# Performance work log

Measured on AMD Instinct MI355X. Metric: run time of the kernel, lower is better.

Reference implementation:

```python
import jax, jax.numpy as jnp
import numpy as np

B, T, D = 64, 512, 1024
V_TAG, V_TYPE = 6, 20
TAG_PAD, TYPE_PAD = 5, 19
E = 2048          # total entity spans in the batch (sliced cascade mode)
MAX_SPAN = 8      # max entity span length


def setup_inputs() -> dict:
    key = jax.random.key(0)
    ks = jax.random.split(key, 12)
    full_hidden = jax.random.normal(ks[0], (B, T, D), dtype=jnp.float32)
    W_tag = jax.random.normal(ks[1], (D, V_TAG), dtype=jnp.float32) * 0.02
    b_tag = jnp.zeros((V_TAG,), jnp.float32)
    W_type = jax.random.normal(ks[2], (D, V_TYPE), dtype=jnp.float32) * 0.02
    b_type = jnp.zeros((V_TYPE,), jnp.float32)
    crf_start = jax.random.normal(ks[3], (V_TAG,), dtype=jnp.float32) * 0.1
    crf_end = jax.random.normal(ks[4], (V_TAG,), dtype=jnp.float32) * 0.1
    crf_trans = jax.random.normal(ks[5], (V_TAG, V_TAG), dtype=jnp.float32) * 0.1
    # ragged sequence lengths (>= MAX_SPAN+1 so all positions/spans are sane)
    seq_lens = jnp.maximum(jax.random.randint(ks[6], (B,), 1, T + 1), MAX_SPAN + 1).astype(jnp.int32)
    tag_ids = jax.random.randint(ks[7], (B, T), 0, V_TAG - 1).astype(jnp.int32)  # exclude pad tag
    ent_sample_ids = jax.random.randint(ks[8], (E,), 0, B).astype(jnp.int32)
    ent_starts = jax.random.randint(ks[9], (E,), 0, T - MAX_SPAN).astype(jnp.int32)
    ent_lens = jax.random.randint(ks[10], (E,), 1, MAX_SPAN + 1)
    ent_ends = (ent_starts + ent_lens).astype(jnp.int32)
    ent_type_ids = jax.random.randint(ks[11], (E,), 0, V_TYPE - 1).astype(jnp.int32)  # exclude pad type
    return dict(full_hidden=full_hidden, W_tag=W_tag, b_tag=b_tag, W_type=W_type,
                b_type=b_type, crf_start=crf_start, crf_end=crf_end, crf_trans=crf_trans,
                tag_ids=tag_ids, seq_lens=seq_lens, ent_sample_ids=ent_sample_ids,
                ent_starts=ent_starts, ent_ends=ent_ends, ent_type_ids=ent_type_ids)


def reference(full_hidden, W_tag, b_tag, W_type, b_type, crf_start, crf_end, crf_trans,
              tag_ids, seq_lens, ent_sample_ids, ent_starts, ent_ends, ent_type_ids):
    mask = jnp.arange(T)[None, :] < seq_lens[:, None]                  # [B,T] bool (tok_mask)
    maskf = mask.astype(full_hidden.dtype)

    # ---- base CRF decoder: tag projection + CRF NLL per sample ----
    tag_feats = full_hidden @ W_tag + b_tag                            # [B,T,V_TAG]

    # gold path score
    emit_scores = jnp.take_along_axis(tag_feats, tag_ids[..., None].astype(jnp.int32), axis=-1)[..., 0]  # [B,T]
    gold = crf_start[tag_ids[:, 0]] + jnp.sum(emit_scores * maskf, axis=1)
    trans_scores = crf_trans[tag_ids[:, :-1], tag_ids[:, 1:]]          # [B,T-1]
    gold = gold + jnp.sum(trans_scores * maskf[:, 1:], axis=1)
    last_tags = tag_ids[jnp.arange(B), seq_lens - 1]
    gold = gold + crf_end[last_tags]

    # log-partition via forward algorithm (log-sum-exp DP, lax.scan over time)
    alpha0 = crf_start[None, :] + tag_feats[:, 0]                      # [B,V]

    def step(alpha, xs):
        emit_t, mask_t = xs                                            # [B,V], [B]
        new = jax.scipy.special.logsumexp(
            alpha[:, :, None] + crf_trans[None, :, :] + emit_t[:, None, :], axis=1)
        return jnp.where(mask_t[:, None], new, alpha), None

    alphaT, _ = jax.lax.scan(step, alpha0,
                             (jnp.swapaxes(tag_feats, 0, 1)[1:], mask.T[1:]))
    logZ = jax.scipy.special.logsumexp(alphaT + crf_end[None, :], axis=-1)  # [B]
    tag_losses = logZ - gold                                           # per-sample CRF NLL

    # ---- sliced cascade: entity-span mean pooling + CE(sum) per sample ----
    type_feats = full_hidden @ W_type + b_type                         # [B,T,V_TYPE]
    csum = jnp.pad(jnp.cumsum(type_feats, axis=1), ((0, 0), (1, 0), (0, 0)))  # [B,T+1,V_TYPE]
    span_sum = csum[ent_sample_ids, ent_ends] - csum[ent_sample_ids, ent_starts]  # [E,V_TYPE]
    span_len = (ent_ends - ent_starts).astype(type_feats.dtype)
    ent_feats = span_sum / span_len[:, None]                           # mean over span
    logp = jax.nn.log_softmax(ent_feats, axis=-1)
    ent_ce = -jnp.take_along_axis(logp, ent_type_ids[:, None].astype(jnp.int32), axis=-1)[:, 0]
    valid = (ent_type_ids != TYPE_PAD).astype(ent_ce.dtype)            # ignore_index
    type_losses = jax.ops.segment_sum(ent_ce * valid, ent_sample_ids, num_segments=B)
    return tag_losses + type_losses                                    # [B]
```

## Files before the change

kernel.cpp:

```cpp
#include <hip/hip_runtime.h>
#include <math.h>
#include <stdint.h>

#define NB  64
#define NT  512
#define ND  1024
#define NVT 6
#define NVY 20
#define TYPE_PAD_V 19
#define NE  2048
#define LOG2E 1.44269504088896340736f
#define LN2   0.69314718055994530942f

typedef float v2f __attribute__((ext_vector_type(2)));

#define OFF_WTT 196608
#define OFF_WS2 217104
#define OFF_G   315408
#define OFF_CE  315472

__global__ __launch_bounds__(256) void k1_tagfeats(const float* __restrict__ H,
                                                   const float* __restrict__ W_tag,
                                                   const float* __restrict__ b_tag,
                                                   const float* __restrict__ W_type,
                                                   float* __restrict__ ws) {
    float* featsT = ws;
    float* WtT    = ws + OFF_WTT;
    if (blockIdx.x < 32) {
        int tid = blockIdx.x * 256 + threadIdx.x;
        for (int i = tid; i < NVY * ND; i += 32 * 256)
            WtT[i] = W_type[(i & (ND - 1)) * NVY + (i >> 10)];
    }

    __shared__ float wlds[NVT][ND];
    for (int i = threadIdx.x; i < ND * NVT; i += 256) {
        int d = i / NVT, v = i % NVT;
        wlds[v][d] = W_tag[i];
    }
    __syncthreads();
    float bt[NVT];
#pragma unroll
    for (int v = 0; v < NVT; ++v) bt[v] = b_tag[v];

    const int lane = threadIdx.x & 63;
    const int wid  = threadIdx.x >> 6;
    const int qw   = lane >> 4;
    const int ql   = lane & 15;
    const int rowBase = blockIdx.x * 32;

#pragma unroll
    for (int it = 0; it < 2; ++it) {
        const int r = rowBase + it * 16 + wid * 4 + qw;
        const float4* hrow = (const float4*)(H + (size_t)r * ND);
        float acc[NVT] = {0.f, 0.f, 0.f, 0.f, 0.f, 0.f};
#pragma unroll
        for (int k = 0; k < 16; ++k) {
            float4 h = hrow[ql + 16 * k];
#pragma unroll
            for (int v = 0; v < NVT; ++v) {
                float4 w = ((const float4*)&wlds[v][0])[ql + 16 * k];
                acc[v] += h.x * w.x + h.y * w.y + h.z * w.z + h.w * w.w;
            }
        }
#pragma unroll
        for (int v = 0; v < NVT; ++v) {
#pragma unroll
            for (int off = 8; off >= 1; off >>= 1)
                acc[v] += __shfl_xor(acc[v], off);
        }
        const int bb = r >> 9;
        const int tt = r & (NT - 1);
#pragma unroll
        for (int v = 0; v < NVT; ++v)
            if (ql == v) featsT[(size_t)tt * 384 + bb * 6 + v] = acc[v] + bt[v];
    }
}

__global__ __launch_bounds__(64) void k2_fused(
    const float* __restrict__ H,
    const float* __restrict__ b_type,
    const float* __restrict__ crf_start,
    const float* __restrict__ crf_end,
    const float* __restrict__ crf_trans,
    const int* __restrict__ tag_ids,
    const int* __restrict__ seq_lens,
    const int* __restrict__ ent_sid,
    const int* __restrict__ ent_st,
    const int* __restrict__ ent_en,
    const int* __restrict__ ent_ty,
    float* __restrict__ ws) {
    const float* featsT = ws;
    const float* WtT    = ws + OFF_WTT;
    float* ws2          = ws + OFF_WS2;
    float* goldv        = ws + OFF_G;
    float* cev          = ws + OFF_CE;
    __shared__ int stag[NT];
    __shared__ float trLp[NVT * NVT];
    const int lane = threadIdx.x;

    if (blockIdx.x < 192) {
        const int c = blockIdx.x / 6;
        const int k = blockIdx.x - 6 * c;
        const int b = lane;
        const int L = seq_lens[b];
        float F[NVT][NVT];
#pragma unroll
        for (int i = 0; i < NVT; ++i)
#pragma unroll
            for (int j = 0; j < NVT; ++j)
                F[i][j] = __builtin_amdgcn_exp2f(crf_trans[i * NVT + j] * LOG2E);
        const char* pf = (const char*)featsT + b * 24;
        v2f Ebuf[16][3];
#pragma unroll
        for (int u = 0; u < 16; ++u) {
            const v2f* p = (const v2f*)(pf + (size_t)(16 * c + 1 + u) * 1536);
            Ebuf[u][0] = p[0]; Ebuf[u][1] = p[1]; Ebuf[u][2] = p[2];
        }
        float v0, v1, v2, v3, v4, v5;
        v0 = (k == 0) ? 1.f : 0.f; v1 = (k == 1) ? 1.f : 0.f; v2 = (k == 2) ? 1.f : 0.f;
        v3 = (k == 3) ? 1.f : 0.f; v4 = (k == 4) ? 1.f : 0.f; v5 = (k == 5) ? 1.f : 0.f;
        int isc = 0;
#pragma unroll
        for (int u = 0; u < 16; ++u) {
            float e0 = __builtin_amdgcn_exp2f(Ebuf[u][0].x * LOG2E);
            float e1 = __builtin_amdgcn_exp2f(Ebuf[u][0].y * LOG2E);
            float e2 = __builtin_amdgcn_exp2f(Ebuf[u][1].x * LOG2E);
            float e3 = __builtin_amdgcn_exp2f(Ebuf[u][1].y * LOG2E);
            float e4 = __builtin_amdgcn_exp2f(Ebuf[u][2].x * LOG2E);
            float e5 = __builtin_amdgcn_exp2f(Ebuf[u][2].y * LOG2E);
            bool ok = (16 * c + 1 + u) < L;
            float g[NVT];
#pragma unroll
            for (int j = 0; j < NVT; ++j) {
                float s = F[0][j] * v0;
                s = __builtin_fmaf(F[1][j], v1, s);
                s = __builtin_fmaf(F[2][j], v2, s);
                s = __builtin_fmaf(F[3][j], v3, s);
                s = __builtin_fmaf(F[4][j], v4, s);
                s = __builtin_fmaf(F[5][j], v5, s);
                g[j] = s;
            }
            v0 = ok ? e0 * g[0] : v0;  v1 = ok ? e1 * g[1] : v1;
            v2 = ok ? e2 * g[2] : v2;  v3 = ok ? e3 * g[3] : v3;
            v4 = ok ? e4 * g[4] : v4;  v5 = ok ? e5 * g[5] : v5;
            if ((u & 3) == 3) {
                float qmax = fmaxf(fmaxf(fmaxf(v0, v1), v2), fmaxf(fmaxf(v3, v4), v5));
                uint32_t eb = __float_as_uint(qmax) >> 23;
                float ri = __uint_as_float((uint32_t)(253 - eb) << 23);
                v0 *= ri; v1 *= ri; v2 *= ri; v3 *= ri; v4 *= ri; v5 *= ri;
                isc += (int)eb - 126;
            }
        }
        float4* dst = (float4*)(ws2 + (((size_t)c * 6 + k) * 64 + b) * 8);
        dst[0] = make_float4(v0, v1, v2, v3);
        dst[1] = make_float4(v4, v5, (float)isc, 0.0f);
    } else if (blockIdx.x < 192 + NB) {
        const int b = blockIdx.x - 192;
        for (int i = lane; i < NT; i += 64) stag[i] = tag_ids[b * NT + i];
        if (lane < NVT * NVT) trLp[lane] = crf_trans[lane];
        __syncthreads();
        const int L = seq_lens[b];
        float g = 0.0f;
#pragma unroll
        for (int k = 0; k < NT / 64; ++k) {
            int t = lane + 64 * k;
            if (t < L) {
                int tg = stag[t];
                g += featsT[(size_t)t * 384 + b * 6 + tg];
                if (t >= 1) g += trLp[stag[t - 1] * NVT + tg];
            }
        }
#pragma unroll
        for (int off = 32; off >= 1; off >>= 1) g += __shfl_xor(g, off);
        if (lane == 0)
            goldv[b] = g + crf_start[stag[0]] + crf_end[stag[L - 1]];
    } else {
        const int e  = blockIdx.x - 192 - NB;
        const int bb = ent_sid[e];
        const int s  = ent_st[e];
        const int en = ent_en[e];
        const int ty = ent_ty[e];
        float4 sv[4];
#pragma unroll
        for (int k = 0; k < 4; ++k) { sv[k].x = 0.f; sv[k].y = 0.f; sv[k].z = 0.f; sv[k].w = 0.f; }
        for (int t = s; t < en; ++t) {
            const float4* hr = (const float4*)(H + ((size_t)bb * NT + t) * ND);
#pragma unroll
            for (int k = 0; k < 4; ++k) {
                float4 h = hr[lane + 64 * k];
                sv[k].x += h.x; sv[k].y += h.y; sv[k].z += h.z; sv[k].w += h.w;
            }
        }
        const float inv = 1.0f / (float)(en - s);
        float f[NVY];
#pragma unroll
        for (int v = 0; v < NVY; ++v) {
            const float4* wv = (const float4*)(WtT + v * ND);
            float p = 0.0f;
#pragma unroll
            for (int k = 0; k < 4; ++k) {
                float4 w = wv[lane + 64 * k];
                p += sv[k].x * w.x + sv[k].y * w.y + sv[k].z * w.z + sv[k].w * w.w;
            }
#pragma unroll
            for (int off = 32; off >= 1; off >>= 1) p += __shfl_xor(p, off);
            f[v] = p * inv + b_type[v];
        }
        float mx = -3.0e38f;
#pragma unroll
        for (int v = 0; v < NVY; ++v) mx = fmaxf(mx, f[v]);
        float sum = 0.0f, goldf = 0.0f;
#pragma unroll
        for (int v = 0; v < NVY; ++v) {
            sum += __expf(f[v] - mx);
            if (v == ty) goldf = f[v];
        }
        float lse = mx + __logf(sum);
        if (lane == 0) cev[e] = (ty != TYPE_PAD_V) ? (lse - goldf) : 0.0f;
    }
}

__global__ __launch_bounds__(256) void k3_final(
    const float* __restrict__ crf_start,
    const float* __restrict__ crf_end,
    const int* __restrict__ ent_sid,
    const float* __restrict__ ws,
    float* __restrict__ out) {
    const float* featsT = ws;
    const float* ws2    = ws + OFF_WS2;
    const float* goldv  = ws + OFF_G;
    const float* cev    = ws + OFF_CE;
    __shared__ float mats[192 * 8];
    __shared__ float part[256];
    const int b   = blockIdx.x;
    const int tid = threadIdx.x;

    {
        const int4*   s4 = (const int4*)ent_sid;
        const float4* c4 = (const float4*)cev;
        float acc = 0.0f;
#pragma unroll
        for (int i = 0; i < 2; ++i) {
            int4   s = s4[tid * 2 + i];
            float4 c = c4[tid * 2 + i];
            acc += (s.x == b) ? c.x : 0.0f;
            acc += (s.y == b) ? c.y : 0.0f;
            acc += (s.z == b) ? c.z : 0.0f;
            acc += (s.w == b) ? c.w : 0.0f;
        }
        part[tid] = acc;
    }
    if (tid < 192) {
        const float4* src = (const float4*)(ws2 + ((size_t)tid * 64 + b) * 8);
        float4 a = src[0], d = src[1];
        ((float4*)&mats[tid * 8])[0] = a;
        ((float4*)&mats[tid * 8])[1] = d;
    }
    __syncthreads();
    if (tid < 128) part[tid] += part[tid + 128];
    __syncthreads();
    if (tid < 64) {
        float v = part[tid] + part[tid + 64];
#pragma unroll
        for (int off = 32; off >= 1; off >>= 1) v += __shfl_xor(v, off);
        if (tid == 0) part[0] = v;
    }
    __syncthreads();

    if (tid < 64) {
        float a0[NVT];
#pragma unroll
        for (int j = 0; j < NVT; ++j) a0[j] = crf_start[j] + featsT[b * 6 + j];
        float m0 = fmaxf(fmaxf(fmaxf(a0[0], a0[1]), a0[2]),
                         fmaxf(fmaxf(a0[3], a0[4]), a0[5]));
        float q[6];
#pragma unroll
        for (int j = 0; j < NVT; ++j)
            q[j] = __builtin_amdgcn_exp2f((a0[j] - m0) * LOG2E);
        float mAcc = m0 * LOG2E;

#pragma unroll 1
        for (int c = 0; c < 32; ++c) {
            const float* m = &mats[c * 48];
            float4 c0a = ((const float4*)m)[0],  c0b = ((const float4*)m)[1];
            float4 c1a = ((const float4*)m)[2],  c1b = ((const float4*)m)[3];
            float4 c2a = ((const float4*)m)[4],  c2b = ((const float4*)m)[5];
            float4 c3a = ((const float4*)m)[6],  c3b = ((const float4*)m)[7];
            float4 c4a = ((const float4*)m)[8],  c4b = ((const float4*)m)[9];
            float4 c5a = ((const float4*)m)[10], c5b = ((const float4*)m)[11];
            float s0 = c0b.z, s1 = c1b.z, s2 = c2b.z, s3 = c3b.z, s4 = c4b.z, s5 = c5b.z;
            float im = fmaxf(fmaxf(fmaxf(s0, s1), fmaxf(s2, s3)), fmaxf(s4, s5));
            float w0 = q[0] * __builtin_amdgcn_exp2f(s0 - im);
            float w1 = q[1] * __builtin_amdgcn_exp2f(s1 - im);
            float w2 = q[2] * __builtin_amdgcn_exp2f(s2 - im);
            float w3 = q[3] * __builtin_amdgcn_exp2f(s3 - im);
            float w4 = q[4] * __builtin_amdgcn_exp2f(s4 - im);
            float w5 = q[5] * __builtin_amdgcn_exp2f(s5 - im);
            float n0 = c0a.x * w0, n1 = c0a.y * w0, n2 = c0a.z * w0,
                  n3 = c0a.w * w0, n4 = c0b.x * w0, n5 = c0b.y * w0;
            n0 = __builtin_fmaf(c1a.x, w1, n0); n1 = __builtin_fmaf(c1a.y, w1, n1);
            n2 = __builtin_fmaf(c1a.z, w1, n2); n3 = __builtin_fmaf(c1a.w, w1, n3);
            n4 = __builtin_fmaf(c1b.x, w1, n4); n5 = __builtin_fmaf(c1b.y, w1, n5);
            n0 = __builtin_fmaf(c2a.x, w2, n0); n1 = __builtin_fmaf(c2a.y, w2, n1);
            n2 = __builtin_fmaf(c2a.z, w2, n2); n3 = __builtin_fmaf(c2a.w, w2, n3);
            n4 = __builtin_fmaf(c2b.x, w2, n4); n5 = __builtin_fmaf(c2b.y, w2, n5);
            n0 = __builtin_fmaf(c3a.x, w3, n0); n1 = __builtin_fmaf(c3a.y, w3, n1);
            n2 = __builtin_fmaf(c3a.z, w3, n2); n3 = __builtin_fmaf(c3a.w, w3, n3);
            n4 = __builtin_fmaf(c3b.x, w3, n4); n5 = __builtin_fmaf(c3b.y, w3, n5);
            n0 = __builtin_fmaf(c4a.x, w4, n0); n1 = __builtin_fmaf(c4a.y, w4, n1);
            n2 = __builtin_fmaf(c4a.z, w4, n2); n3 = __builtin_fmaf(c4a.w, w4, n3);
            n4 = __builtin_fmaf(c4b.x, w4, n4); n5 = __builtin_fmaf(c4b.y, w4, n5);
            n0 = __builtin_fmaf(c5a.x, w5, n0); n1 = __builtin_fmaf(c5a.y, w5, n1);
            n2 = __builtin_fmaf(c5a.z, w5, n2); n3 = __builtin_fmaf(c5a.w, w5, n3);
            n4 = __builtin_fmaf(c5b.x, w5, n4); n5 = __builtin_fmaf(c5b.y, w5, n5);
            float qm = fmaxf(fmaxf(fmaxf(n0, n1), n2), fmaxf(fmaxf(n3, n4), n5));
            uint32_t eb = __float_as_uint(qm) >> 23;
            float ri = __uint_as_float((uint32_t)(253 - eb) << 23);
            q[0] = n0 * ri; q[1] = n1 * ri; q[2] = n2 * ri;
            q[3] = n3 * ri; q[4] = n4 * ri; q[5] = n5 * ri;
            mAcc += im + (float)((int)eb - 126);
        }

        float zs = 0.0f;
#pragma unroll
        for (int j = 0; j < NVT; ++j)
            zs += q[j] * __builtin_amdgcn_exp2f(crf_end[j] * LOG2E);
        float logZ = LN2 * (mAcc + __builtin_amdgcn_logf(zs));
        if (tid == 0)
            out[b] = logZ - goldv[b] + part[0];
    }
}

extern "C" void kernel_launch(void* const* d_in, const int* in_sizes, int n_in,
                              void* d_out, int out_size, void* d_ws, size_t ws_size,
                              hipStream_t stream) {
    const float* H         = (const float*)d_in[0];
    const float* W_tag     = (const float*)d_in[1];
    const float* b_tag     = (const float*)d_in[2];
    const float* W_type    = (const float*)d_in[3];
    const float* b_type    = (const float*)d_in[4];
    const float* crf_start = (const float*)d_in[5];
    const float* crf_end   = (const float*)d_in[6];
    const float* crf_trans = (const float*)d_in[7];
    const int* tag_ids     = (const int*)d_in[8];
    const int* seq_lens    = (const int*)d_in[9];
    const int* ent_sid     = (const int*)d_in[10];
    const int* ent_st      = (const int*)d_in[11];
    const int* ent_en      = (const int*)d_in[12];
    const int* ent_ty      = (const int*)d_in[13];
    float* out = (float*)d_out;
    float* ws  = (float*)d_ws;

    hipLaunchKernelGGL(k1_tagfeats, dim3(1024), dim3(256), 0, stream,
                       H, W_tag, b_tag, W_type, ws);
    hipLaunchKernelGGL(k2_fused, dim3(192 + NB + NE), dim3(64), 0, stream,
                       H, b_type, crf_start, crf_end, crf_trans,
                       tag_ids, seq_lens, ent_sid, ent_st, ent_en, ent_ty, ws);
    hipLaunchKernelGGL(k3_final, dim3(NB), dim3(256), 0, stream,
                       crf_start, crf_end, ent_sid, ws, out);
}
```

Before: 52.16 us.

## Move entity span pooling into first kernel and drop W_type transpose

The entity-span pooling and type cross-entropy move out of the CRF kernel and into the tag-projection kernel as extra blocks, one wave per entity and four entities per block. W_type is read directly in its original row-major layout, with each lane owning 16 contiguous hidden dims and accumulating all 20 logits, so the transpose pass into the workspace goes away. The goal is to let the entity work overlap the bandwidth-bound tag projection and to shorten the CRF kernel's critical path. In exchange there are 20 cross-lane reductions per entity and higher register use, and the wlds shared memory is also allocated for the entity blocks.

```diff
diff --git a/kernel.cpp b/kernel.cpp
--- a/kernel.cpp
+++ b/kernel.cpp
@@ -14,86 +14,149 @@
 
 typedef float v2f __attribute__((ext_vector_type(2)));
 
-#define OFF_WTT 196608
 #define OFF_WS2 217104
 #define OFF_G   315408
 #define OFF_CE  315472
 
-__global__ __launch_bounds__(256) void k1_tagfeats(const float* __restrict__ H,
-                                                   const float* __restrict__ W_tag,
-                                                   const float* __restrict__ b_tag,
-                                                   const float* __restrict__ W_type,
-                                                   float* __restrict__ ws) {
+__global__ __launch_bounds__(256) void k1_fused(const float* __restrict__ H,
+                                                const float* __restrict__ W_tag,
+                                                const float* __restrict__ b_tag,
+                                                const float* __restrict__ W_type,
+                                                const float* __restrict__ b_type,
+                                                const int* __restrict__ ent_sid,
+                                                const int* __restrict__ ent_st,
+                                                const int* __restrict__ ent_en,
+                                                const int* __restrict__ ent_ty,
+                                                float* __restrict__ ws) {
     float* featsT = ws;
-    float* WtT    = ws + OFF_WTT;
-    if (blockIdx.x < 32) {
-        int tid = blockIdx.x * 256 + threadIdx.x;
-        for (int i = tid; i < NVY * ND; i += 32 * 256)
-            WtT[i] = W_type[(i & (ND - 1)) * NVY + (i >> 10)];
-    }
-
+    float* cev    = ws + OFF_CE;
     __shared__ float wlds[NVT][ND];
-    for (int i = threadIdx.x; i < ND * NVT; i += 256) {
-        int d = i / NVT, v = i % NVT;
-        wlds[v][d] = W_tag[i];
-    }
-    __syncthreads();
-    float bt[NVT];
-#pragma unroll
-    for (int v = 0; v < NVT; ++v) bt[v] = b_tag[v];
-
     const int lane = threadIdx.x & 63;
     const int wid  = threadIdx.x >> 6;
-    const int qw   = lane >> 4;
-    const int ql   = lane & 15;
-    const int rowBase = blockIdx.x * 32;
-
-#pragma unroll
-    for (int it = 0; it < 2; ++it) {
-        const int r = rowBase + it * 16 + wid * 4 + qw;
-        const float4* hrow = (const float4*)(H + (size_t)r * ND);
-        float acc[NVT] = {0.f, 0.f, 0.f, 0.f, 0.f, 0.f};
-#pragma unroll
-        for (int k = 0; k < 16; ++k) {
-            float4 h = hrow[ql + 16 * k];
+
+    if (blockIdx.x < 1024) {
+        for (int i = threadIdx.x; i < ND * NVT; i += 256) {
+            int d = i / NVT, v = i % NVT;
+            wlds[v][d] = W_tag[i];
+        }
+        __syncthreads();
+        float bt[NVT];
+#pragma unroll
+        for (int v = 0; v < NVT; ++v) bt[v] = b_tag[v];
+
+        const int qw = lane >> 4;
+        const int ql = lane & 15;
+        const int rowBase = blockIdx.x * 32;
+#pragma unroll
+        for (int it = 0; it < 2; ++it) {
+            const int r = rowBase + it * 16 + wid * 4 + qw;
+            const float4* hrow = (const float4*)(H + (size_t)r * ND);
+            float acc[NVT] = {0.f, 0.f, 0.f, 0.f, 0.f, 0.f};
+#pragma unroll
+            for (int k = 0; k < 16; ++k) {
+                float4 h = hrow[ql + 16 * k];
+#pragma unroll
+                for (int v = 0; v < NVT; ++v) {
+                    float4 w = ((const float4*)&wlds[v][0])[ql + 16 * k];
+                    acc[v] += h.x * w.x + h.y * w.y + h.z * w.z + h.w * w.w;
+                }
+            }
 #pragma unroll
             for (int v = 0; v < NVT; ++v) {
-                float4 w = ((const float4*)&wlds[v][0])[ql + 16 * k];
-                acc[v] += h.x * w.x + h.y * w.y + h.z * w.z + h.w * w.w;
-            }
-        }
-#pragma unroll
-        for (int v = 0; v < NVT; ++v) {
-#pragma unroll
-            for (int off = 8; off >= 1; off >>= 1)
-                acc[v] += __shfl_xor(acc[v], off);
-        }
-        const int bb = r >> 9;
-        const int tt = r & (NT - 1);
-#pragma unroll
-        for (int v = 0; v < NVT; ++v)
-            if (ql == v) featsT[(size_t)tt * 384 + bb * 6 + v] = acc[v] + bt[v];
+#pragma unroll
+                for (int off = 8; off >= 1; off >>= 1)
+                    acc[v] += __shfl_xor(acc[v], off);
+            }
+            const int bb = r >> 9;
+            const int tt = r & (NT - 1);
+#pragma unroll
+            for (int v = 0; v < NVT; ++v)
+                if (ql == v) featsT[(size_t)tt * 384 + bb * 6 + v] = acc[v] + bt[v];
+        }
+    } else {
+        const int e  = (blockIdx.x - 1024) * 4 + wid;
+        const int bb = ent_sid[e];
+        const int s  = ent_st[e];
+        const int en = ent_en[e];
+        const int ty = ent_ty[e];
+        float4 sv0 = {0,0,0,0}, sv1 = {0,0,0,0}, sv2 = {0,0,0,0}, sv3 = {0,0,0,0};
+        for (int t = s; t < en; ++t) {
+            const float4* hr = (const float4*)(H + ((size_t)bb * NT + t) * ND);
+            float4 h0 = hr[lane * 4], h1 = hr[lane * 4 + 1],
+                   h2 = hr[lane * 4 + 2], h3 = hr[lane * 4 + 3];
+            sv0.x += h0.x; sv0.y += h0.y; sv0.z += h0.z; sv0.w += h0.w;
+            sv1.x += h1.x; sv1.y += h1.y; sv1.z += h1.z; sv1.w += h1.w;
+            sv2.x += h2.x; sv2.y += h2.y; sv2.z += h2.z; sv2.w += h2.w;
+            sv3.x += h3.x; sv3.y += h3.y; sv3.z += h3.z; sv3.w += h3.w;
+        }
+        float svd[16];
+        svd[0] = sv0.x; svd[1] = sv0.y; svd[2]  = sv0.z; svd[3]  = sv0.w;
+        svd[4] = sv1.x; svd[5] = sv1.y; svd[6]  = sv1.z; svd[7]  = sv1.w;
+        svd[8] = sv2.x; svd[9] = sv2.y; svd[10] = sv2.z; svd[11] = sv2.w;
+        svd[12] = sv3.x; svd[13] = sv3.y; svd[14] = sv3.z; svd[15] = sv3.w;
+
+        float f[NVY];
+#pragma unroll
+        for (int v = 0; v < NVY; ++v) f[v] = 0.0f;
+#pragma unroll
+        for (int r = 0; r < 16; ++r) {
+            const float4* w4 = (const float4*)(W_type + ((size_t)lane * 16 + r) * NVY);
+            float4 wa = w4[0], wb = w4[1], wc = w4[2], wd = w4[3], we = w4[4];
+            float hv = svd[r];
+            f[0]  = __builtin_fmaf(hv, wa.x, f[0]);
+            f[1]  = __builtin_fmaf(hv, wa.y, f[1]);
+            f[2]  = __builtin_fmaf(hv, wa.z, f[2]);
+            f[3]  = __builtin_fmaf(hv, wa.w, f[3]);
+            f[4]  = __builtin_fmaf(hv, wb.x, f[4]);
+            f[5]  = __builtin_fmaf(hv, wb.y, f[5]);
+            f[6]  = __builtin_fmaf(hv, wb.z, f[6]);
+            f[7]  = __builtin_fmaf(hv, wb.w, f[7]);
+            f[8]  = __builtin_fmaf(hv, wc.x, f[8]);
+            f[9]  = __builtin_fmaf(hv, wc.y, f[9]);
+            f[10] = __builtin_fmaf(hv, wc.z, f[10]);
+            f[11] = __builtin_fmaf(hv, wc.w, f[11]);
+            f[12] = __builtin_fmaf(hv, wd.x, f[12]);
+            f[13] = __builtin_fmaf(hv, wd.y, f[13]);
+            f[14] = __builtin_fmaf(hv, wd.z, f[14]);
+            f[15] = __builtin_fmaf(hv, wd.w, f[15]);
+            f[16] = __builtin_fmaf(hv, we.x, f[16]);
+            f[17] = __builtin_fmaf(hv, we.y, f[17]);
+            f[18] = __builtin_fmaf(hv, we.z, f[18]);
+            f[19] = __builtin_fmaf(hv, we.w, f[19]);
+        }
+#pragma unroll
+        for (int off = 32; off >= 1; off >>= 1) {
+#pragma unroll
+            for (int v = 0; v < NVY; ++v) f[v] += __shfl_xor(f[v], off);
+        }
+        const float inv = 1.0f / (float)(en - s);
+        float mx = -3.0e38f;
+#pragma unroll
+        for (int v = 0; v < NVY; ++v) {
+            f[v] = f[v] * inv + b_type[v];
+            mx = fmaxf(mx, f[v]);
+        }
+        float sum = 0.0f, goldf = 0.0f;
+#pragma unroll
+        for (int v = 0; v < NVY; ++v) {
+            sum += __expf(f[v] - mx);
+            if (v == ty) goldf = f[v];
+        }
+        float lse = mx + __logf(sum);
+        if (lane == 0) cev[e] = (ty != TYPE_PAD_V) ? (lse - goldf) : 0.0f;
     }
 }
 
 __global__ __launch_bounds__(64) void k2_fused(
-    const float* __restrict__ H,
-    const float* __restrict__ b_type,
     const float* __restrict__ crf_start,
     const float* __restrict__ crf_end,
     const float* __restrict__ crf_trans,
     const int* __restrict__ tag_ids,
     const int* __restrict__ seq_lens,
-    const int* __restrict__ ent_sid,
-    const int* __restrict__ ent_st,
-    const int* __restrict__ ent_en,
-    const int* __restrict__ ent_ty,
     float* __restrict__ ws) {
     const float* featsT = ws;
-    const float* WtT    = ws + OFF_WTT;
     float* ws2          = ws + OFF_WS2;
     float* goldv        = ws + OFF_G;
-    float* cev          = ws + OFF_CE;
     __shared__ int stag[NT];
     __shared__ float trLp[NVT * NVT];
     const int lane = threadIdx.x;
@@ -154,7 +217,7 @@
         float4* dst = (float4*)(ws2 + (((size_t)c * 6 + k) * 64 + b) * 8);
         dst[0] = make_float4(v0, v1, v2, v3);
         dst[1] = make_float4(v4, v5, (float)isc, 0.0f);
-    } else if (blockIdx.x < 192 + NB) {
+    } else {
         const int b = blockIdx.x - 192;
         for (int i = lane; i < NT; i += 64) stag[i] = tag_ids[b * NT + i];
         if (lane < NVT * NVT) trLp[lane] = crf_trans[lane];
@@ -174,49 +237,6 @@
         for (int off = 32; off >= 1; off >>= 1) g += __shfl_xor(g, off);
         if (lane == 0)
             goldv[b] = g + crf_start[stag[0]] + crf_end[stag[L - 1]];
-    } else {
-        const int e  = blockIdx.x - 192 - NB;
-        const int bb = ent_sid[e];
-        const int s  = ent_st[e];
-        const int en = ent_en[e];
-        const int ty = ent_ty[e];
-        float4 sv[4];
-#pragma unroll
-        for (int k = 0; k < 4; ++k) { sv[k].x = 0.f; sv[k].y = 0.f; sv[k].z = 0.f; sv[k].w = 0.f; }
-        for (int t = s; t < en; ++t) {
-            const float4* hr = (const float4*)(H + ((size_t)bb * NT + t) * ND);
-#pragma unroll
-            for (int k = 0; k < 4; ++k) {
-                float4 h = hr[lane + 64 * k];
-                sv[k].x += h.x; sv[k].y += h.y; sv[k].z += h.z; sv[k].w += h.w;
-            }
-        }
-        const float inv = 1.0f / (float)(en - s);
-        float f[NVY];
-#pragma unroll
-        for (int v = 0; v < NVY; ++v) {
-            const float4* wv = (const float4*)(WtT + v * ND);
-            float p = 0.0f;
-#pragma unroll
-            for (int k = 0; k < 4; ++k) {
-                float4 w = wv[lane + 64 * k];
-                p += sv[k].x * w.x + sv[k].y * w.y + sv[k].z * w.z + sv[k].w * w.w;
-            }
-#pragma unroll
-            for (int off = 32; off >= 1; off >>= 1) p += __shfl_xor(p, off);
-            f[v] = p * inv + b_type[v];
-        }
-        float mx = -3.0e38f;
-#pragma unroll
-        for (int v = 0; v < NVY; ++v) mx = fmaxf(mx, f[v]);
-        float sum = 0.0f, goldf = 0.0f;
-#pragma unroll
-        for (int v = 0; v < NVY; ++v) {
-            sum += __expf(f[v] - mx);
-            if (v == ty) goldf = f[v];
-        }
-        float lse = mx + __logf(sum);
-        if (lane == 0) cev[e] = (ty != TYPE_PAD_V) ? (lse - goldf) : 0.0f;
     }
 }
 
@@ -351,11 +371,11 @@
     float* out = (float*)d_out;
     float* ws  = (float*)d_ws;
 
-    hipLaunchKernelGGL(k1_tagfeats, dim3(1024), dim3(256), 0, stream,
-                       H, W_tag, b_tag, W_type, ws);
-    hipLaunchKernelGGL(k2_fused, dim3(192 + NB + NE), dim3(64), 0, stream,
-                       H, b_type, crf_start, crf_end, crf_trans,
-                       tag_ids, seq_lens, ent_sid, ent_st, ent_en, ent_ty, ws);
+    hipLaunchKernelGGL(k1_fused, dim3(1024 + NE / 4), dim3(256), 0, stream,
+                       H, W_tag, b_tag, W_type, b_type,
+                       ent_sid, ent_st, ent_en, ent_ty, ws);
+    hipLaunchKernelGGL(k2_fused, dim3(192 + NB), dim3(64), 0, stream,
+                       crf_start, crf_end, crf_trans, tag_ids, seq_lens, ws);
     hipLaunchKernelGGL(k3_final, dim3(NB), dim3(256), 0, stream,
                        crf_start, crf_end, ent_sid, ws, out);
 }
```

Result: slower. 72.86 us (+39.7%).
